# Optimization experiments

Hardware: AMD Instinct MI355X
Metric: run time of the kernel (lower is better)

## Reference

```python
import jax, jax.numpy as jnp
import numpy as np

NUM_HEADS = 16
HEAD_DIM = 64
D_MODEL = NUM_HEADS * HEAD_DIM  # 1024
TOP_K_TILES = 8
TILE_SIZE = 16


def setup_inputs() -> dict:
    key = jax.random.key(0)
    kx, kq, kk, kv, ko = jax.random.split(key, 5)
    B, S = 2, 2048
    scale = 1.0 / np.sqrt(D_MODEL)
    return {
        "x": jax.random.normal(kx, (B, S, D_MODEL), dtype=jnp.float32),
        "wq": jax.random.normal(kq, (D_MODEL, NUM_HEADS * HEAD_DIM), dtype=jnp.float32) * scale,
        "wk": jax.random.normal(kk, (D_MODEL, NUM_HEADS * HEAD_DIM), dtype=jnp.float32) * scale,
        "wv": jax.random.normal(kv, (D_MODEL, NUM_HEADS * HEAD_DIM), dtype=jnp.float32) * scale,
        "wo": jax.random.normal(ko, (NUM_HEADS * HEAD_DIM, D_MODEL), dtype=jnp.float32) * scale,
    }


def reference(x, wq, wk, wv, wo):
    B, S, _ = x.shape
    H, D = NUM_HEADS, HEAD_DIM
    q = (x @ wq).reshape(B, S, H, D)
    k = (x @ wk).reshape(B, S, H, D)
    v = (x @ wv).reshape(B, S, H, D)
    logits = jnp.einsum('bqhd,bkhd->bhqk', q, k) / jnp.sqrt(jnp.float32(D))
    causal = jnp.tril(jnp.ones((S, S), dtype=bool))
    logits = jnp.where(causal[None, None, :, :], logits, jnp.float32(-1e10))
    weights = jax.nn.softmax(logits, axis=-1)  # [B,H,S,S]

    # tile pooling + top-k on the last query row (auxiliary output, cached in original)
    last_token_probs = weights[:, :, -1, :]  # [B,H,S]
    pad_len = (TILE_SIZE - S % TILE_SIZE) % TILE_SIZE
    if pad_len > 0:
        last_token_probs = jnp.pad(last_token_probs, ((0, 0), (0, 0), (0, pad_len)))
    num_tiles = last_token_probs.shape[-1] // TILE_SIZE
    tile_scores = last_token_probs.reshape(B, H, num_tiles, TILE_SIZE).max(axis=-1)
    _, top_tile_indices = jax.lax.top_k(tile_scores, TOP_K_TILES)  # side output
    del top_tile_indices  # original stores in a global cache; not returned

    out = jnp.einsum('bhqk,bkhd->bqhd', weights, v).reshape(B, S, H * D)
    return out @ wo
```

## Files before the change

kernel.cpp:

```cpp
#include <hip/hip_runtime.h>
#include <hip/hip_bf16.h>

#define NUM_HEADS 16
#define HEAD_DIM 64
#define DMODEL 1024
#define SEQ 2048
#define BATCH 2
#define MROWS (BATCH*SEQ)

typedef __bf16 bf16;
typedef __bf16 bf16x4 __attribute__((ext_vector_type(4)));
typedef __bf16 bf16x8 __attribute__((ext_vector_type(8)));
typedef float f32x4 __attribute__((ext_vector_type(4)));

#define MFMA16(a, b, c) __builtin_amdgcn_mfma_f32_16x16x32_bf16((a), (b), (c), 0, 0, 0)

#define QSCALE 0.1803368801111444f

__device__ __forceinline__ float fast_exp2(float x) {
    float r;
    asm("v_exp_f32 %0, %1" : "=v"(r) : "v"(x));
    return r;
}

__device__ __forceinline__ void gld16(const void* g, void* l) {
    __builtin_amdgcn_global_load_lds(
        (const __attribute__((address_space(1))) void*)g,
        (__attribute__((address_space(3))) void*)l, 16, 0, 0);
}


__global__ __launch_bounds__(256) void cvt_f32_bf16(const float* __restrict__ in,
                                                    bf16* __restrict__ out, int n4) {
    int i = blockIdx.x * 256 + threadIdx.x;
    if (i >= n4) return;
    float4 v = *(const float4*)(in + (size_t)i * 4);
    bf16x4 o = { (bf16)v.x, (bf16)v.y, (bf16)v.z, (bf16)v.w };
    *(bf16x4*)(out + (size_t)i * 4) = o;
}

__global__ __launch_bounds__(256) void cvt_trans(const float* __restrict__ w0, const float* __restrict__ w1,
                                                 const float* __restrict__ w2, const float* __restrict__ w3,
                                                 bf16* __restrict__ o0, bf16* __restrict__ o1,
                                                 bf16* __restrict__ o2, bf16* __restrict__ o3) {
    const float* w = blockIdx.z == 0 ? w0 : blockIdx.z == 1 ? w1 : blockIdx.z == 2 ? w2 : w3;
    bf16* o = blockIdx.z == 0 ? o0 : blockIdx.z == 1 ? o1 : blockIdx.z == 2 ? o2 : o3;
    __shared__ bf16 tile[64][65];
    int k0 = blockIdx.y * 64, n0 = blockIdx.x * 64;
    int tc = threadIdx.x & 63;
    int tr0 = threadIdx.x >> 6;
#pragma unroll
    for (int i = 0; i < 16; i++) {
        int r = tr0 + i * 4;
        tile[r][tc] = (bf16)w[(size_t)(k0 + r) * DMODEL + n0 + tc];
    }
    __syncthreads();
#pragma unroll
    for (int i = 0; i < 16; i++) {
        int r = tr0 + i * 4;
        o[(size_t)(n0 + r) * DMODEL + k0 + tc] = tile[tc][r];
    }
}


#define BM 128
#define BN 128
#define BK 32

__device__ __forceinline__ void gemm_core(const bf16* __restrict__ A, const bf16* __restrict__ Bt,
                                          int m0, int n0, int Kdim,
                                          bf16* As, bf16* Bs, f32x4 acc[4][4]) {
    int t = threadIdx.x;
    int lane = t & 63;
    int wave = t >> 6;
    int wm = (wave >> 1) * 64;
    int wn = (wave & 1) * 64;
#pragma unroll
    for (int mf = 0; mf < 4; mf++)
#pragma unroll
        for (int nf = 0; nf < 4; nf++) acc[mf][nf] = (f32x4){0.f, 0.f, 0.f, 0.f};

    int arow = lane & 15, kg = lane >> 4;

    for (int k0 = 0; k0 < Kdim; k0 += BK) {
        __syncthreads();
#pragma unroll
        for (int it = 0; it < 2; it++) {
            int chunk = it * 256 + t;
            int rr = chunk >> 2, cc = chunk & 3;
            gld16(A + (size_t)(m0 + rr) * Kdim + k0 + cc * 8, As + chunk * 8);
            gld16(Bt + (size_t)(n0 + rr) * Kdim + k0 + cc * 8, Bs + chunk * 8);
        }
        __syncthreads();
        bf16x8 af[4], bfr[4];
#pragma unroll
        for (int mf = 0; mf < 4; mf++)
            af[mf] = *(const bf16x8*)(As + (wm + mf * 16 + arow) * BK + kg * 8);
#pragma unroll
        for (int nf = 0; nf < 4; nf++)
            bfr[nf] = *(const bf16x8*)(Bs + (wn + nf * 16 + arow) * BK + kg * 8);
#pragma unroll
        for (int mf = 0; mf < 4; mf++)
#pragma unroll
            for (int nf = 0; nf < 4; nf++)
                acc[mf][nf] = MFMA16(af[mf], bfr[nf], acc[mf][nf]);
    }
}

__global__ __launch_bounds__(256) void gemm_qkv(const bf16* __restrict__ xb,
                                                const bf16* __restrict__ wqT, const bf16* __restrict__ wkT,
                                                const bf16* __restrict__ wvT,
                                                bf16* __restrict__ Qh, bf16* __restrict__ Kh,
                                                bf16* __restrict__ Vt) {
    __shared__ __attribute__((aligned(16))) bf16 As[BM * BK];
    __shared__ __attribute__((aligned(16))) bf16 Bs[BN * BK];
    int z = blockIdx.z;
    const bf16* Bt = z == 0 ? wqT : z == 1 ? wkT : wvT;
    int m0 = blockIdx.y * BM, n0 = blockIdx.x * BN;
    f32x4 acc[4][4];
    gemm_core(xb, Bt, m0, n0, DMODEL, As, Bs, acc);

    int lane = threadIdx.x & 63, wave = threadIdx.x >> 6;
    int wm = (wave >> 1) * 64, wn = (wave & 1) * 64;
    int col0 = n0 + wn + (lane & 15);
    int row0 = m0 + wm + (lane >> 4) * 4;
    if (z < 2) {
        bf16* O = z == 0 ? Qh : Kh;
        float scl = z == 0 ? QSCALE : 1.0f;
#pragma unroll
        for (int mf = 0; mf < 4; mf++)
#pragma unroll
            for (int nf = 0; nf < 4; nf++) {
                int n = col0 + nf * 16;
                int mb = row0 + mf * 16;
                int hh = n >> 6, d = n & 63;
#pragma unroll
                for (int i2 = 0; i2 < 4; i2++) {
                    int m = mb + i2;
                    int bb = m >> 11, s = m & 2047;
                    O[(((size_t)bb * NUM_HEADS + hh) * SEQ + s) * HEAD_DIM + d] =
                        (bf16)(acc[mf][nf][i2] * scl);
                }
            }
    } else {
#pragma unroll
        for (int mf = 0; mf < 4; mf++)
#pragma unroll
            for (int nf = 0; nf < 4; nf++) {
                int n = col0 + nf * 16;
                int m = row0 + mf * 16;
                int b = m >> 11, s = m & 2047;
                int h = n >> 6, d = n & 63;
                bf16x4 pack = { (bf16)acc[mf][nf][0], (bf16)acc[mf][nf][1],
                                (bf16)acc[mf][nf][2], (bf16)acc[mf][nf][3] };
                *(bf16x4*)(Vt + ((size_t)(b * NUM_HEADS + h) * HEAD_DIM + d) * SEQ + s) = pack;
            }
    }
}

__global__ __launch_bounds__(256) void gemm_outp(const bf16* __restrict__ at,
                                                 const bf16* __restrict__ woT,
                                                 float* __restrict__ out) {
    __shared__ __attribute__((aligned(16))) bf16 As[BM * BK];
    __shared__ __attribute__((aligned(16))) bf16 Bs[BN * BK];
    int m0 = blockIdx.y * BM, n0 = blockIdx.x * BN;
    f32x4 acc[4][4];
    gemm_core(at, woT, m0, n0, DMODEL, As, Bs, acc);

    int lane = threadIdx.x & 63, wave = threadIdx.x >> 6;
    int wm = (wave >> 1) * 64, wn = (wave & 1) * 64;
    int col0 = n0 + wn + (lane & 15);
    int row0 = m0 + wm + (lane >> 4) * 4;
#pragma unroll
    for (int mf = 0; mf < 4; mf++)
#pragma unroll
        for (int nf = 0; nf < 4; nf++) {
            int n = col0 + nf * 16;
            int mb = row0 + mf * 16;
#pragma unroll
            for (int i2 = 0; i2 < 4; i2++)
                out[(size_t)(mb + i2) * DMODEL + n] = acc[mf][nf][i2];
        }
}

__global__ __launch_bounds__(256) void attn_kernel(const bf16* __restrict__ Qh, const bf16* __restrict__ Kh,
                                                   const bf16* __restrict__ Vt, bf16* __restrict__ attn) {
    __shared__ __attribute__((aligned(16))) bf16 Kl[2 * 64 * 64];
    __shared__ __attribute__((aligned(16))) bf16 Vl[2 * 64 * 64];
    __shared__ __attribute__((aligned(16))) bf16 Pl[4 * 16 * 64];
    int id = blockIdx.x;
    int xcd = id & 7, slot = id >> 3;
    int bh4 = slot >> 4;
    int pairIdx = slot & 15;
    int hb = xcd * 4 + bh4;
    int b = hb >> 4, h = hb & 15;
    int t = threadIdx.x, lane = t & 63, wave = t >> 6;
    int l15 = lane & 15, lg = lane >> 4;

    const bf16* Qb = Qh + ((size_t)(b * NUM_HEADS + h) * SEQ) * HEAD_DIM;
    const bf16* Kb = Kh + ((size_t)(b * NUM_HEADS + h) * SEQ) * HEAD_DIM;
    const bf16* Vb = Vt + ((size_t)(b * NUM_HEADS + h) * HEAD_DIM) * SEQ;

    char* Pw = (char*)Pl + wave * 2048;
    int swz = (l15 & 7) << 4;

    auto STAGE = [&](int bufi, int kv0n) {
#pragma unroll
        for (int j = 0; j < 2; j++) {
            int c = j * 256 + t;
            int L = (c * 16) ^ (((c >> 3) & 7) << 4);
            int row = c >> 3, cole = (L & 127) >> 1;
            gld16(Kb + (size_t)(kv0n + row) * HEAD_DIM + cole,
                  (char*)Kl + (size_t)bufi * 8192 + c * 16);
            gld16(Vb + (size_t)row * SEQ + kv0n + cole,
                  (char*)Vl + (size_t)bufi * 8192 + c * 16);
        }
    };

#pragma unroll 1
    for (int seg = 0; seg < 2; seg++) {
        int qt = seg ? (31 - pairIdx) : pairIdx;
        int q0w = qt * 64 + wave * 16;
        int nkt = qt + 1;

        bf16x8 qf[2];
#pragma unroll
        for (int ks = 0; ks < 2; ks++)
            qf[ks] = *(const bf16x8*)(Qb + (size_t)(q0w + l15) * HEAD_DIM + ks * 32 + lg * 8);

        f32x4 oacc[4];
#pragma unroll
        for (int df = 0; df < 4; df++) oacc[df] = (f32x4){0.f, 0.f, 0.f, 0.f};
        float mrun = -1e30f, lrun = 0.f;

        STAGE(0, 0);
        __syncthreads();
        int buf = 0;

        for (int kt = 0; kt < nkt; kt++) {
            int kv0 = kt * 64;
            if (kt + 1 < nkt) STAGE(buf ^ 1, kv0 + 64);

            const char* KL = (const char*)Kl + (size_t)buf * 8192;
            const char* VL = (const char*)Vl + (size_t)buf * 8192;
            f32x4 st[4];
            __builtin_amdgcn_s_setprio(1);
#pragma unroll
            for (int cf = 0; cf < 4; cf++) {
                bf16x8 kfr[2];
#pragma unroll
                for (int ks = 0; ks < 2; ks++) {
                    int off = ((cf * 16 + l15) * 128 + ks * 64 + lg * 16) ^ swz;
                    kfr[ks] = *(const bf16x8*)(KL + off);
                }
                st[cf] = (f32x4){0.f, 0.f, 0.f, 0.f};
#pragma unroll
                for (int ks = 0; ks < 2; ks++)
                    st[cf] = MFMA16(kfr[ks], qf[ks], st[cf]);
            }
            __builtin_amdgcn_s_setprio(0);
            if (kt == nkt - 1) {
                int qrow = q0w + l15;
#pragma unroll
                for (int cf = 0; cf < 4; cf++)
#pragma unroll
                    for (int i = 0; i < 4; i++) {
                        int kv = kv0 + cf * 16 + lg * 4 + i;
                        if (kv > qrow) st[cf][i] = -1e30f;
                    }
            }
            float m01 = fmaxf(fmaxf(st[0][0], st[0][1]), fmaxf(st[0][2], st[0][3]));
            float m23 = fmaxf(fmaxf(st[1][0], st[1][1]), fmaxf(st[1][2], st[1][3]));
            float m45 = fmaxf(fmaxf(st[2][0], st[2][1]), fmaxf(st[2][2], st[2][3]));
            float m67 = fmaxf(fmaxf(st[3][0], st[3][1]), fmaxf(st[3][2], st[3][3]));
            float mx = fmaxf(fmaxf(m01, m23), fmaxf(m45, m67));
            mx = fmaxf(mx, __shfl_xor(mx, 16, 64));
            mx = fmaxf(mx, __shfl_xor(mx, 32, 64));
            if (!__all(mx <= mrun + 8.0f)) {
                float mnew = fmaxf(mrun, mx);
                float alpha = fast_exp2(mrun - mnew);
                float av[4];
#pragma unroll
                for (int i = 0; i < 4; i++) av[i] = __shfl(alpha, lg * 4 + i, 64);
#pragma unroll
                for (int df = 0; df < 4; df++)
#pragma unroll
                    for (int i = 0; i < 4; i++) oacc[df][i] *= av[i];
                lrun *= alpha;
                mrun = mnew;
            }
            float psc[4];
            bf16x4 pb[4];
#pragma unroll
            for (int cf = 0; cf < 4; cf++) {
                float p0 = fast_exp2(st[cf][0] - mrun);
                float p1 = fast_exp2(st[cf][1] - mrun);
                float p2 = fast_exp2(st[cf][2] - mrun);
                float p3 = fast_exp2(st[cf][3] - mrun);
                psc[cf] = (p0 + p1) + (p2 + p3);
                pb[cf][0] = (bf16)p0; pb[cf][1] = (bf16)p1;
                pb[cf][2] = (bf16)p2; pb[cf][3] = (bf16)p3;
            }
            float ps = (psc[0] + psc[1]) + (psc[2] + psc[3]);
            ps += __shfl_xor(ps, 16, 64);
            ps += __shfl_xor(ps, 32, 64);
            lrun += ps;
#pragma unroll
            for (int cf = 0; cf < 4; cf++) {
                int off = (l15 * 128 + cf * 32 + lg * 8) ^ swz;
                *(bf16x4*)(Pw + off) = pb[cf];
            }
            bf16x8 pa[2];
#pragma unroll
            for (int ks = 0; ks < 2; ks++) {
                int off = (l15 * 128 + ks * 64 + lg * 16) ^ swz;
                pa[ks] = *(const bf16x8*)(Pw + off);
            }
            __builtin_amdgcn_s_setprio(1);
#pragma unroll
            for (int ks = 0; ks < 2; ks++)
#pragma unroll
                for (int df = 0; df < 4; df++) {
                    int off = ((df * 16 + l15) * 128 + ks * 64 + lg * 16) ^ swz;
                    bf16x8 bv = *(const bf16x8*)(VL + off);
                    oacc[df] = MFMA16(pa[ks], bv, oacc[df]);
                }
            __builtin_amdgcn_s_setprio(0);

            __syncthreads();
            buf ^= 1;
        }

        float lrec = 1.0f / lrun;
        float lv[4];
#pragma unroll
        for (int i = 0; i < 4; i++) lv[i] = __shfl(lrec, lg * 4 + i, 64);
#pragma unroll
        for (int df = 0; df < 4; df++)
#pragma unroll
            for (int i = 0; i < 4; i++) {
                int qrow = q0w + lg * 4 + i;
                int d = df * 16 + l15;
                attn[((size_t)(b * SEQ + qrow)) * DMODEL + h * HEAD_DIM + d] = (bf16)(oacc[df][i] * lv[i]);
            }
    }
}


extern "C" void kernel_launch(void* const* d_in, const int* in_sizes, int n_in,
                              void* d_out, int out_size, void* d_ws, size_t ws_size,
                              hipStream_t stream) {
    const float* x  = (const float*)d_in[0];
    const float* wq = (const float*)d_in[1];
    const float* wk = (const float*)d_in[2];
    const float* wv = (const float*)d_in[3];
    const float* wo = (const float*)d_in[4];
    float* out = (float*)d_out;

    char* w = (char*)d_ws;
    bf16* xb  = (bf16*)(w);
    bf16* wqT = (bf16*)(w + (8ull  << 20));
    bf16* wkT = (bf16*)(w + (10ull << 20));
    bf16* wvT = (bf16*)(w + (12ull << 20));
    bf16* woT = (bf16*)(w + (14ull << 20));
    bf16* Qh  = (bf16*)(w + (16ull << 20));
    bf16* Kh  = (bf16*)(w + (24ull << 20));
    bf16* Vt  = (bf16*)(w + (32ull << 20));
    bf16* at  = (bf16*)(w + (40ull << 20));

    cvt_f32_bf16<<<(MROWS * DMODEL / 4 + 255) / 256, 256, 0, stream>>>(x, xb, MROWS * DMODEL / 4);
    cvt_trans<<<dim3(16, 16, 4), 256, 0, stream>>>(wq, wk, wv, wo, wqT, wkT, wvT, woT);
    gemm_qkv<<<dim3(DMODEL / BN, MROWS / BM, 3), 256, 0, stream>>>(xb, wqT, wkT, wvT, Qh, Kh, Vt);
    attn_kernel<<<dim3(512, 1, 1), 256, 0, stream>>>(Qh, Kh, Vt, at);
    gemm_outp<<<dim3(DMODEL / BN, MROWS / BM), 256, 0, stream>>>(at, woT, out);
}
```

Before: 119.1 us.

## Triple-buffer LDS staging with explicit vmcnt waits in GEMMs and attention

Both the projection GEMM core and the attention KV loop now stage tiles into a three-deep LDS ring, prefetching two tiles ahead. Full __syncthreads is replaced by explicit s_waitcnt vmcnt counts plus a raw barrier, so loads for later tiles can stay in flight across the barrier. The GEMM also gains setprio around its MFMA block. The cost is more LDS per block (the GEMMs triple theirs, attention grows by a third), which may reduce occupancy, and the hand-counted vmcnt values must match the number of outstanding loads per stage.

```diff
diff --git a/kernel.cpp b/kernel.cpp
--- a/kernel.cpp
+++ b/kernel.cpp
@@ -16,6 +16,9 @@
 #define MFMA16(a, b, c) __builtin_amdgcn_mfma_f32_16x16x32_bf16((a), (b), (c), 0, 0, 0)
 
 #define QSCALE 0.1803368801111444f
+
+#define VMW(N) asm volatile("s_waitcnt vmcnt(" #N ")" ::: "memory")
+#define BARRIER() do { __builtin_amdgcn_s_barrier(); __builtin_amdgcn_sched_barrier(0); } while (0)
 
 __device__ __forceinline__ float fast_exp2(float x) {
     float r;
@@ -81,29 +84,46 @@
         for (int nf = 0; nf < 4; nf++) acc[mf][nf] = (f32x4){0.f, 0.f, 0.f, 0.f};
 
     int arow = lane & 15, kg = lane >> 4;
-
-    for (int k0 = 0; k0 < Kdim; k0 += BK) {
-        __syncthreads();
+    int rr = t >> 2, cc = t & 3;
+    int nk = Kdim / BK;
+
+    auto STAGE = [&](int bufi, int ks) {
+        int k0 = ks * BK;
 #pragma unroll
         for (int it = 0; it < 2; it++) {
             int chunk = it * 256 + t;
-            int rr = chunk >> 2, cc = chunk & 3;
-            gld16(A + (size_t)(m0 + rr) * Kdim + k0 + cc * 8, As + chunk * 8);
-            gld16(Bt + (size_t)(n0 + rr) * Kdim + k0 + cc * 8, Bs + chunk * 8);
-        }
-        __syncthreads();
+            int r2 = it * 64 + rr;
+            gld16(A + (size_t)(m0 + r2) * Kdim + k0 + cc * 8, As + bufi * (BM * BK) + chunk * 8);
+            gld16(Bt + (size_t)(n0 + r2) * Kdim + k0 + cc * 8, Bs + bufi * (BM * BK) + chunk * 8);
+        }
+    };
+
+    STAGE(0, 0);
+    if (nk > 1) { STAGE(1, 1); VMW(4); } else { VMW(0); }
+    BARRIER();
+
+    for (int ks = 0; ks < nk; ks++) {
+        if (ks + 2 < nk) STAGE((ks + 2) % 3, ks + 2);
+        const bf16* Ab = As + (ks % 3) * (BM * BK);
+        const bf16* Bb = Bs + (ks % 3) * (BM * BK);
         bf16x8 af[4], bfr[4];
 #pragma unroll
         for (int mf = 0; mf < 4; mf++)
-            af[mf] = *(const bf16x8*)(As + (wm + mf * 16 + arow) * BK + kg * 8);
+            af[mf] = *(const bf16x8*)(Ab + (wm + mf * 16 + arow) * BK + kg * 8);
 #pragma unroll
         for (int nf = 0; nf < 4; nf++)
-            bfr[nf] = *(const bf16x8*)(Bs + (wn + nf * 16 + arow) * BK + kg * 8);
+            bfr[nf] = *(const bf16x8*)(Bb + (wn + nf * 16 + arow) * BK + kg * 8);
+        __builtin_amdgcn_s_setprio(1);
 #pragma unroll
         for (int mf = 0; mf < 4; mf++)
 #pragma unroll
             for (int nf = 0; nf < 4; nf++)
                 acc[mf][nf] = MFMA16(af[mf], bfr[nf], acc[mf][nf]);
+        __builtin_amdgcn_s_setprio(0);
+        if (ks + 1 < nk) {
+            if (ks + 2 < nk) VMW(4); else VMW(0);
+        }
+        BARRIER();
     }
 }
 
@@ -112,8 +132,8 @@
                                                 const bf16* __restrict__ wvT,
                                                 bf16* __restrict__ Qh, bf16* __restrict__ Kh,
                                                 bf16* __restrict__ Vt) {
-    __shared__ __attribute__((aligned(16))) bf16 As[BM * BK];
-    __shared__ __attribute__((aligned(16))) bf16 Bs[BN * BK];
+    __shared__ __attribute__((aligned(16))) bf16 As[3 * BM * BK];
+    __shared__ __attribute__((aligned(16))) bf16 Bs[3 * BN * BK];
     int z = blockIdx.z;
     const bf16* Bt = z == 0 ? wqT : z == 1 ? wkT : wvT;
     int m0 = blockIdx.y * BM, n0 = blockIdx.x * BN;
@@ -161,8 +181,8 @@
 __global__ __launch_bounds__(256) void gemm_outp(const bf16* __restrict__ at,
                                                  const bf16* __restrict__ woT,
                                                  float* __restrict__ out) {
-    __shared__ __attribute__((aligned(16))) bf16 As[BM * BK];
-    __shared__ __attribute__((aligned(16))) bf16 Bs[BN * BK];
+    __shared__ __attribute__((aligned(16))) bf16 As[3 * BM * BK];
+    __shared__ __attribute__((aligned(16))) bf16 Bs[3 * BN * BK];
     int m0 = blockIdx.y * BM, n0 = blockIdx.x * BN;
     f32x4 acc[4][4];
     gemm_core(at, woT, m0, n0, DMODEL, As, Bs, acc);
@@ -185,8 +205,8 @@
 
 __global__ __launch_bounds__(256) void attn_kernel(const bf16* __restrict__ Qh, const bf16* __restrict__ Kh,
                                                    const bf16* __restrict__ Vt, bf16* __restrict__ attn) {
-    __shared__ __attribute__((aligned(16))) bf16 Kl[2 * 64 * 64];
-    __shared__ __attribute__((aligned(16))) bf16 Vl[2 * 64 * 64];
+    __shared__ __attribute__((aligned(16))) bf16 Kl[3 * 64 * 64];
+    __shared__ __attribute__((aligned(16))) bf16 Vl[3 * 64 * 64];
     __shared__ __attribute__((aligned(16))) bf16 Pl[4 * 16 * 64];
     int id = blockIdx.x;
     int xcd = id & 7, slot = id >> 3;
@@ -234,15 +254,15 @@
         float mrun = -1e30f, lrun = 0.f;
 
         STAGE(0, 0);
-        __syncthreads();
-        int buf = 0;
+        if (nkt > 1) { STAGE(1, 64); VMW(4); } else { VMW(0); }
+        BARRIER();
 
         for (int kt = 0; kt < nkt; kt++) {
             int kv0 = kt * 64;
-            if (kt + 1 < nkt) STAGE(buf ^ 1, kv0 + 64);
-
-            const char* KL = (const char*)Kl + (size_t)buf * 8192;
-            const char* VL = (const char*)Vl + (size_t)buf * 8192;
+            if (kt + 2 < nkt) STAGE((kt + 2) % 3, kv0 + 128);
+
+            const char* KL = (const char*)Kl + (size_t)(kt % 3) * 8192;
+            const char* VL = (const char*)Vl + (size_t)(kt % 3) * 8192;
             f32x4 st[4];
             __builtin_amdgcn_s_setprio(1);
 #pragma unroll
@@ -327,8 +347,10 @@
                 }
             __builtin_amdgcn_s_setprio(0);
 
-            __syncthreads();
-            buf ^= 1;
+            if (kt + 1 < nkt) {
+                if (kt + 2 < nkt) VMW(4); else VMW(0);
+            }
+            BARRIER();
         }
 
         float lrec = 1.0f / lrun;
```

After: 146.9 us. 23.4% more time.

## Split attention KV loop across two wave groups and merge softmax partials

Applied to the files above, without the earlier changes.

The attention kernel now launches 512 threads per block. Two groups of four waves each process alternating KV tiles for the same query strip, staged through a four-deep LDS ring buffer. At the end, the partial output, running max and running sum of group 0 are written to shared memory and combined with group 1's using the online-softmax rescale before the bf16 store. This doubles the waves working on each query tile to shorten the serial KV loop, at the cost of a cross-group merge, more LDS per block, and extra barriers.

```diff
diff --git a/kernel.cpp b/kernel.cpp
--- a/kernel.cpp
+++ b/kernel.cpp
@@ -183,11 +183,11 @@
         }
 }
 
-__global__ __launch_bounds__(256) void attn_kernel(const bf16* __restrict__ Qh, const bf16* __restrict__ Kh,
-                                                   const bf16* __restrict__ Vt, bf16* __restrict__ attn) {
-    __shared__ __attribute__((aligned(16))) bf16 Kl[2 * 64 * 64];
-    __shared__ __attribute__((aligned(16))) bf16 Vl[2 * 64 * 64];
-    __shared__ __attribute__((aligned(16))) bf16 Pl[4 * 16 * 64];
+__global__ __launch_bounds__(512, 4) void attn_kernel(const bf16* __restrict__ Qh, const bf16* __restrict__ Kh,
+                                                      const bf16* __restrict__ Vt, bf16* __restrict__ attn) {
+    __shared__ __attribute__((aligned(16))) bf16 Kl[4 * 64 * 64];
+    __shared__ __attribute__((aligned(16))) bf16 Vl[4 * 64 * 64];
+    __shared__ __attribute__((aligned(16))) bf16 Pl[8 * 16 * 64];
     int id = blockIdx.x;
     int xcd = id & 7, slot = id >> 3;
     int bh4 = slot >> 4;
@@ -196,6 +196,8 @@
     int b = hb >> 4, h = hb & 15;
     int t = threadIdx.x, lane = t & 63, wave = t >> 6;
     int l15 = lane & 15, lg = lane >> 4;
+    int strip = wave & 3;
+    int gp = wave >> 2;
 
     const bf16* Qb = Qh + ((size_t)(b * NUM_HEADS + h) * SEQ) * HEAD_DIM;
     const bf16* Kb = Kh + ((size_t)(b * NUM_HEADS + h) * SEQ) * HEAD_DIM;
@@ -203,25 +205,25 @@
 
     char* Pw = (char*)Pl + wave * 2048;
     int swz = (l15 & 7) << 4;
-
-    auto STAGE = [&](int bufi, int kv0n) {
-#pragma unroll
-        for (int j = 0; j < 2; j++) {
-            int c = j * 256 + t;
-            int L = (c * 16) ^ (((c >> 3) & 7) << 4);
-            int row = c >> 3, cole = (L & 127) >> 1;
-            gld16(Kb + (size_t)(kv0n + row) * HEAD_DIM + cole,
-                  (char*)Kl + (size_t)bufi * 8192 + c * 16);
-            gld16(Vb + (size_t)row * SEQ + kv0n + cole,
-                  (char*)Vl + (size_t)bufi * 8192 + c * 16);
-        }
+    float* M = (float*)Kl;
+
+    int sc = t;
+    int sL = (sc * 16) ^ (((sc >> 3) & 7) << 4);
+    int srow = sc >> 3, scole = (sL & 127) >> 1;
+
+    auto STAGE = [&](int kt) {
+        int kv0n = kt * 64;
+        int bi = kt & 3;
+        gld16(Kb + (size_t)(kv0n + srow) * HEAD_DIM + scole, (char*)Kl + bi * 8192 + sc * 16);
+        gld16(Vb + (size_t)srow * SEQ + kv0n + scole,        (char*)Vl + bi * 8192 + sc * 16);
     };
 
 #pragma unroll 1
     for (int seg = 0; seg < 2; seg++) {
         int qt = seg ? (31 - pairIdx) : pairIdx;
-        int q0w = qt * 64 + wave * 16;
+        int q0w = qt * 64 + strip * 16;
         int nkt = qt + 1;
+        int imax = (nkt + 1) >> 1;
 
         bf16x8 qf[2];
 #pragma unroll
@@ -233,116 +235,149 @@
         for (int df = 0; df < 4; df++) oacc[df] = (f32x4){0.f, 0.f, 0.f, 0.f};
         float mrun = -1e30f, lrun = 0.f;
 
-        STAGE(0, 0);
-        __syncthreads();
-        int buf = 0;
-
-        for (int kt = 0; kt < nkt; kt++) {
-            int kv0 = kt * 64;
-            if (kt + 1 < nkt) STAGE(buf ^ 1, kv0 + 64);
-
-            const char* KL = (const char*)Kl + (size_t)buf * 8192;
-            const char* VL = (const char*)Vl + (size_t)buf * 8192;
-            f32x4 st[4];
-            __builtin_amdgcn_s_setprio(1);
-#pragma unroll
-            for (int cf = 0; cf < 4; cf++) {
-                bf16x8 kfr[2];
+        STAGE(0);
+        if (nkt > 1) STAGE(1);
+        __syncthreads();
+
+#pragma unroll 1
+        for (int j = 0; j < imax; j++) {
+            int kt = 2 * j + gp;
+            int s0 = 2 * j + 2;
+            if (s0 < nkt) STAGE(s0);
+            if (s0 + 1 < nkt) STAGE(s0 + 1);
+
+            if (kt <= qt) {
+                int kv0 = kt * 64;
+                const char* KL = (const char*)Kl + (kt & 3) * 8192;
+                const char* VL = (const char*)Vl + (kt & 3) * 8192;
+                f32x4 st[4];
+                __builtin_amdgcn_s_setprio(1);
+#pragma unroll
+                for (int cf = 0; cf < 4; cf++) {
+                    bf16x8 kfr[2];
+#pragma unroll
+                    for (int ks = 0; ks < 2; ks++) {
+                        int off = ((cf * 16 + l15) * 128 + ks * 64 + lg * 16) ^ swz;
+                        kfr[ks] = *(const bf16x8*)(KL + off);
+                    }
+                    st[cf] = (f32x4){0.f, 0.f, 0.f, 0.f};
+#pragma unroll
+                    for (int ks = 0; ks < 2; ks++)
+                        st[cf] = MFMA16(kfr[ks], qf[ks], st[cf]);
+                }
+                __builtin_amdgcn_s_setprio(0);
+                if (kt == qt) {
+                    int qrow = q0w + l15;
+#pragma unroll
+                    for (int cf = 0; cf < 4; cf++)
+#pragma unroll
+                        for (int i = 0; i < 4; i++) {
+                            int kv = kv0 + cf * 16 + lg * 4 + i;
+                            if (kv > qrow) st[cf][i] = -1e30f;
+                        }
+                }
+                float m01 = fmaxf(fmaxf(st[0][0], st[0][1]), fmaxf(st[0][2], st[0][3]));
+                float m23 = fmaxf(fmaxf(st[1][0], st[1][1]), fmaxf(st[1][2], st[1][3]));
+                float m45 = fmaxf(fmaxf(st[2][0], st[2][1]), fmaxf(st[2][2], st[2][3]));
+                float m67 = fmaxf(fmaxf(st[3][0], st[3][1]), fmaxf(st[3][2], st[3][3]));
+                float mx = fmaxf(fmaxf(m01, m23), fmaxf(m45, m67));
+                mx = fmaxf(mx, __shfl_xor(mx, 16, 64));
+                mx = fmaxf(mx, __shfl_xor(mx, 32, 64));
+                if (!__all(mx <= mrun + 8.0f)) {
+                    float mnew = fmaxf(mrun, mx);
+                    float alpha = fast_exp2(mrun - mnew);
+                    float av[4];
+#pragma unroll
+                    for (int i = 0; i < 4; i++) av[i] = __shfl(alpha, lg * 4 + i, 64);
+#pragma unroll
+                    for (int df = 0; df < 4; df++)
+#pragma unroll
+                        for (int i = 0; i < 4; i++) oacc[df][i] *= av[i];
+                    lrun *= alpha;
+                    mrun = mnew;
+                }
+                float psc[4];
+                bf16x4 pb[4];
+#pragma unroll
+                for (int cf = 0; cf < 4; cf++) {
+                    float p0 = fast_exp2(st[cf][0] - mrun);
+                    float p1 = fast_exp2(st[cf][1] - mrun);
+                    float p2 = fast_exp2(st[cf][2] - mrun);
+                    float p3 = fast_exp2(st[cf][3] - mrun);
+                    psc[cf] = (p0 + p1) + (p2 + p3);
+                    pb[cf][0] = (bf16)p0; pb[cf][1] = (bf16)p1;
+                    pb[cf][2] = (bf16)p2; pb[cf][3] = (bf16)p3;
+                }
+                float ps = (psc[0] + psc[1]) + (psc[2] + psc[3]);
+                ps += __shfl_xor(ps, 16, 64);
+                ps += __shfl_xor(ps, 32, 64);
+                lrun += ps;
+#pragma unroll
+                for (int cf = 0; cf < 4; cf++) {
+                    int off = (l15 * 128 + cf * 32 + lg * 8) ^ swz;
+                    *(bf16x4*)(Pw + off) = pb[cf];
+                }
+                bf16x8 pa[2];
 #pragma unroll
                 for (int ks = 0; ks < 2; ks++) {
-                    int off = ((cf * 16 + l15) * 128 + ks * 64 + lg * 16) ^ swz;
-                    kfr[ks] = *(const bf16x8*)(KL + off);
-                }
-                st[cf] = (f32x4){0.f, 0.f, 0.f, 0.f};
+                    int off = (l15 * 128 + ks * 64 + lg * 16) ^ swz;
+                    pa[ks] = *(const bf16x8*)(Pw + off);
+                }
+                __builtin_amdgcn_s_setprio(1);
 #pragma unroll
                 for (int ks = 0; ks < 2; ks++)
-                    st[cf] = MFMA16(kfr[ks], qf[ks], st[cf]);
+#pragma unroll
+                    for (int df = 0; df < 4; df++) {
+                        int off = ((df * 16 + l15) * 128 + ks * 64 + lg * 16) ^ swz;
+                        bf16x8 bv = *(const bf16x8*)(VL + off);
+                        oacc[df] = MFMA16(pa[ks], bv, oacc[df]);
+                    }
+                __builtin_amdgcn_s_setprio(0);
             }
-            __builtin_amdgcn_s_setprio(0);
-            if (kt == nkt - 1) {
-                int qrow = q0w + l15;
-#pragma unroll
-                for (int cf = 0; cf < 4; cf++)
-#pragma unroll
-                    for (int i = 0; i < 4; i++) {
-                        int kv = kv0 + cf * 16 + lg * 4 + i;
-                        if (kv > qrow) st[cf][i] = -1e30f;
-                    }
+            __syncthreads();
+        }
+
+        if (gp == 0) {
+#pragma unroll
+            for (int df = 0; df < 4; df++)
+#pragma unroll
+                for (int i = 0; i < 4; i++)
+                    M[strip * 1040 + (lg * 4 + i) * 65 + df * 16 + l15] = oacc[df][i];
+            if (lg == 0) {
+                M[4160 + strip * 16 + l15] = mrun;
+                M[4224 + strip * 16 + l15] = lrun;
             }
-            float m01 = fmaxf(fmaxf(st[0][0], st[0][1]), fmaxf(st[0][2], st[0][3]));
-            float m23 = fmaxf(fmaxf(st[1][0], st[1][1]), fmaxf(st[1][2], st[1][3]));
-            float m45 = fmaxf(fmaxf(st[2][0], st[2][1]), fmaxf(st[2][2], st[2][3]));
-            float m67 = fmaxf(fmaxf(st[3][0], st[3][1]), fmaxf(st[3][2], st[3][3]));
-            float mx = fmaxf(fmaxf(m01, m23), fmaxf(m45, m67));
-            mx = fmaxf(mx, __shfl_xor(mx, 16, 64));
-            mx = fmaxf(mx, __shfl_xor(mx, 32, 64));
-            if (!__all(mx <= mrun + 8.0f)) {
-                float mnew = fmaxf(mrun, mx);
-                float alpha = fast_exp2(mrun - mnew);
-                float av[4];
-#pragma unroll
-                for (int i = 0; i < 4; i++) av[i] = __shfl(alpha, lg * 4 + i, 64);
-#pragma unroll
-                for (int df = 0; df < 4; df++)
-#pragma unroll
-                    for (int i = 0; i < 4; i++) oacc[df][i] *= av[i];
-                lrun *= alpha;
-                mrun = mnew;
+        }
+        __syncthreads();
+        if (gp == 1) {
+            float mA = M[4160 + strip * 16 + l15];
+            float lA = M[4224 + strip * 16 + l15];
+            float ms = fmaxf(mrun, mA);
+            float aB = fast_exp2(mrun - ms);
+            float aA = fast_exp2(mA - ms);
+            float lrec = 1.0f / (lrun * aB + lA * aA);
+            if (lg == 0) {
+                M[4288 + strip * 16 + l15] = aA * lrec;
+                M[4352 + strip * 16 + l15] = aB * lrec;
             }
-            float psc[4];
-            bf16x4 pb[4];
-#pragma unroll
-            for (int cf = 0; cf < 4; cf++) {
-                float p0 = fast_exp2(st[cf][0] - mrun);
-                float p1 = fast_exp2(st[cf][1] - mrun);
-                float p2 = fast_exp2(st[cf][2] - mrun);
-                float p3 = fast_exp2(st[cf][3] - mrun);
-                psc[cf] = (p0 + p1) + (p2 + p3);
-                pb[cf][0] = (bf16)p0; pb[cf][1] = (bf16)p1;
-                pb[cf][2] = (bf16)p2; pb[cf][3] = (bf16)p3;
-            }
-            float ps = (psc[0] + psc[1]) + (psc[2] + psc[3]);
-            ps += __shfl_xor(ps, 16, 64);
-            ps += __shfl_xor(ps, 32, 64);
-            lrun += ps;
-#pragma unroll
-            for (int cf = 0; cf < 4; cf++) {
-                int off = (l15 * 128 + cf * 32 + lg * 8) ^ swz;
-                *(bf16x4*)(Pw + off) = pb[cf];
-            }
-            bf16x8 pa[2];
-#pragma unroll
-            for (int ks = 0; ks < 2; ks++) {
-                int off = (l15 * 128 + ks * 64 + lg * 16) ^ swz;
-                pa[ks] = *(const bf16x8*)(Pw + off);
-            }
-            __builtin_amdgcn_s_setprio(1);
-#pragma unroll
-            for (int ks = 0; ks < 2; ks++)
-#pragma unroll
-                for (int df = 0; df < 4; df++) {
-                    int off = ((df * 16 + l15) * 128 + ks * 64 + lg * 16) ^ swz;
-                    bf16x8 bv = *(const bf16x8*)(VL + off);
-                    oacc[df] = MFMA16(pa[ks], bv, oacc[df]);
-                }
-            __builtin_amdgcn_s_setprio(0);
-
-            __syncthreads();
-            buf ^= 1;
-        }
-
-        float lrec = 1.0f / lrun;
-        float lv[4];
-#pragma unroll
-        for (int i = 0; i < 4; i++) lv[i] = __shfl(lrec, lg * 4 + i, 64);
-#pragma unroll
-        for (int df = 0; df < 4; df++)
-#pragma unroll
-            for (int i = 0; i < 4; i++) {
-                int qrow = q0w + lg * 4 + i;
-                int d = df * 16 + l15;
-                attn[((size_t)(b * SEQ + qrow)) * DMODEL + h * HEAD_DIM + d] = (bf16)(oacc[df][i] * lv[i]);
-            }
+        }
+        __syncthreads();
+        if (gp == 1) {
+#pragma unroll
+            for (int df = 0; df < 4; df++)
+#pragma unroll
+                for (int i = 0; i < 4; i++) {
+                    int r = lg * 4 + i;
+                    float cA = M[4288 + strip * 16 + r];
+                    float cB = M[4352 + strip * 16 + r];
+                    float oA = M[strip * 1040 + r * 65 + df * 16 + l15];
+                    int qrow = qt * 64 + strip * 16 + r;
+                    int d = df * 16 + l15;
+                    attn[((size_t)(b * SEQ + qrow)) * DMODEL + h * HEAD_DIM + d] =
+                        (bf16)(oacc[df][i] * cB + oA * cA);
+                }
+        }
+        __syncthreads();
     }
 }
 
@@ -371,6 +406,6 @@
     cvt_f32_bf16<<<(MROWS * DMODEL / 4 + 255) / 256, 256, 0, stream>>>(x, xb, MROWS * DMODEL / 4);
     cvt_trans<<<dim3(16, 16, 4), 256, 0, stream>>>(wq, wk, wv, wo, wqT, wkT, wvT, woT);
     gemm_qkv<<<dim3(DMODEL / BN, MROWS / BM, 3), 256, 0, stream>>>(xb, wqT, wkT, wvT, Qh, Kh, Vt);
-    attn_kernel<<<dim3(512, 1, 1), 256, 0, stream>>>(Qh, Kh, Vt, at);
+    attn_kernel<<<dim3(512, 1, 1), 512, 0, stream>>>(Qh, Kh, Vt, at);
     gemm_outp<<<dim3(DMODEL / BN, MROWS / BM), 256, 0, stream>>>(at, woT, out);
 }
```

Result: faster. 111.2 us (-6.6%).
